# Optimization experiments

Measured on AMD Instinct MI355X. Metric: run time of the kernel, lower is better.

The kernel has to match this reference:

```python
import jax, jax.numpy as jnp
import numpy as np

CONFIDENCE = 0.1
EPS = 1e-3  # keras BatchNormalization default epsilon
B, H, W, C = 4, 64, 64, 256


def setup_inputs() -> dict:
    key = jax.random.key(0)
    ks = jax.random.split(key, 6)
    return {
        "x": jax.random.normal(ks[0], (B, H, W, C), jnp.float32),
        "ca_gamma": jnp.ones((C,), jnp.float32),
        "ca_beta": jnp.zeros((C,), jnp.float32),
        "ca_mean": jnp.zeros((C,), jnp.float32),
        "ca_var": jnp.ones((C,), jnp.float32),
        "wq": jax.random.normal(ks[1], (C, C), jnp.float32) * 0.05,
        "wk": jax.random.normal(ks[2], (C, C), jnp.float32) * 0.05,
        "wv": jax.random.normal(ks[3], (C, C), jnp.float32) * 0.05,
        "wp": jax.random.normal(ks[4], (C, C), jnp.float32) * 0.05,
        "bn_gamma": jnp.ones((C,), jnp.float32),
        "bn_beta": jnp.zeros((C,), jnp.float32),
        "bn_mean": jnp.zeros((C,), jnp.float32),
        "bn_var": jnp.ones((C,), jnp.float32),
        "w_qkv": jax.random.normal(ks[5], (C, 3), jnp.float32) * 0.05,
    }


def _bn(x, g, b, m, v):
    # keras BatchNormalization, inference mode
    return (x - m) * jax.lax.rsqrt(v + EPS) * g + b


def reference(x, ca_gamma, ca_beta, ca_mean, ca_var, wq, wk, wv, wp,
              bn_gamma, bn_beta, bn_mean, bn_var, w_qkv):
    b, h, w, c = x.shape
    # ---- ChannelAttention (TRACER Channel_Tracer; dropout = identity at inference) ----
    gap = x.mean(axis=(1, 2))                         # [B, C] global average pool
    gn = _bn(gap, ca_gamma, ca_beta, ca_mean, ca_var)  # [B, C]
    q = gn @ wq                                        # 1x1 conv on 1x1 map == matmul
    k = gn @ wk
    v = gn @ wv
    logits = q[:, :, None] * k[:, None, :]             # [B, C, C], head_dim = 1
    score = jax.nn.softmax(logits, axis=-1)
    att = jnp.einsum('bij,bj->bi', score, v)           # [B, C]
    cmask = jax.nn.sigmoid(att @ wp)                   # [B, C] channel mask (alpha)
    ca_out = x * cmask[:, None, None, :] + x           # residual channel re-weighting
    # ---- UnionAttention spatial part ----
    co = _bn(ca_out, bn_gamma, bn_beta, bn_mean, bn_var)
    thr = jnp.percentile(cmask, CONFIDENCE * 100.0, axis=-1,
                         keepdims=True, method='linear')  # [B, 1]
    pmask = jnp.where(cmask > thr, cmask, 0.0)          # percentile masking
    co = co * pmask[:, None, None, :]
    qkv = jnp.einsum('bhwc,cf->bhwf', co, w_qkv)        # [B, H, W, 3] fused q/k/v 1x1 conv
    n = h * w
    qs = qkv[..., 0].reshape(b, n)                      # [B, N], head_dim = 1
    ks_ = qkv[..., 1].reshape(b, n)
    vs = qkv[..., 2].reshape(b, n)
    sl = qs[:, :, None] * ks_[:, None, :]               # [B, N, N] scores (outer product)
    sw = jax.nn.softmax(sl, axis=-1)
    sa = jnp.einsum('bij,bj->bi', sw, vs)               # [B, N]
    return qkv[..., 2:3] + sa.reshape(b, h, w, 1)       # v + attention, [B, H, W, 1]
```

## Files before the change

### kernel.cpp

```cpp
#include <hip/hip_runtime.h>

#define EPS 1e-3f

#define OFF_PGAP   0
#define OFF_PART   65536
#define OFF_A      163840
#define OFF_BIAS   164864
#define OFF_QS     164880
#define OFF_KS     181264
#define OFF_VS     197648

__global__ __launch_bounds__(256) void k_gap(const float* __restrict__ x,
                                             const float* __restrict__ wq,
                                             const float* __restrict__ wk,
                                             const float* __restrict__ wv,
                                             const float* __restrict__ wp,
                                             float* __restrict__ pgap) {
    __shared__ float4 red[256];
    int blk = blockIdx.x;
    int t = threadIdx.x;

    const float* wmat = (blk < 64) ? wq : (blk < 128) ? wk : (blk < 192) ? wv : wp;
    float4 wv4 = *(const float4*)(wmat + (size_t)(blk & 63) * 1024 + 4 * t);

    int cg = t & 63;
    int pg = t >> 6;
    const float* xp = x + ((size_t)blk * 64 + pg * 16) * 256 + 4 * cg;
    float4 s = make_float4(0.f, 0.f, 0.f, 0.f);
    #pragma unroll
    for (int u = 0; u < 16; ++u) {
        float4 v = *(const float4*)(xp + (size_t)u * 256);
        s.x += v.x; s.y += v.y; s.z += v.z; s.w += v.w;
    }
    red[pg * 64 + cg] = s;
    asm volatile("" :: "v"(wv4.x), "v"(wv4.y), "v"(wv4.z), "v"(wv4.w));
    __syncthreads();
    if (t < 64) {
        float4 a = red[t], b4 = red[64 + t], c4 = red[128 + t], d4 = red[192 + t];
        float4 o = make_float4(a.x + b4.x + c4.x + d4.x,
                               a.y + b4.y + c4.y + d4.y,
                               a.z + b4.z + c4.z + d4.z,
                               a.w + b4.w + c4.w + d4.w);
        *(float4*)(pgap + blk * 256 + 4 * t) = o;
    }
}

__global__ __launch_bounds__(256) void k_qkvmat(
    const float* __restrict__ pgap,
    const float* __restrict__ cag, const float* __restrict__ cab,
    const float* __restrict__ cam, const float* __restrict__ cav,
    const float* __restrict__ wq, const float* __restrict__ wk,
    const float* __restrict__ wv,
    float* __restrict__ part)
{
    __shared__ float gpart[4][8][4];
    __shared__ float gn_s[4][8];
    int blk = blockIdx.x;
    int m = blk >> 5;
    int g = blk & 31;
    int r0 = g * 8;
    int t = threadIdx.x;
    const float* W = (m == 0) ? wq : (m == 1) ? wk : wv;

    if (t < 128) {
        int b = t >> 5, row = (t >> 2) & 7, p = t & 3;
        const float* pgp = pgap + ((size_t)(b * 64 + p * 16)) * 256 + r0 + row;
        float s = 0.f;
        #pragma unroll
        for (int ch = 0; ch < 16; ++ch) s += pgp[(size_t)ch * 256];
        gpart[b][row][p] = s;
    }
    __syncthreads();
    if (t < 32) {
        int b = t >> 3, row = t & 7;
        float gsum = gpart[b][row][0] + gpart[b][row][1]
                   + gpart[b][row][2] + gpart[b][row][3];
        float gv = gsum * (1.0f / 4096.0f);
        int c = r0 + row;
        float sc = cag[c] * rsqrtf(cav[c] + EPS);
        gn_s[b][row] = gv * sc + (cab[c] - cam[c] * sc);
    }
    __syncthreads();

    float a0 = 0.f, a1 = 0.f, a2 = 0.f, a3 = 0.f;
    const float* wp_ = W + (size_t)r0 * 256 + t;
    #pragma unroll
    for (int row = 0; row < 8; ++row) {
        float w = wp_[(size_t)row * 256];
        a0 = fmaf(gn_s[0][row], w, a0);
        a1 = fmaf(gn_s[1][row], w, a1);
        a2 = fmaf(gn_s[2][row], w, a2);
        a3 = fmaf(gn_s[3][row], w, a3);
    }
    float* o = part + (size_t)(m * 32 + g) * 1024 + t;
    o[0] = a0; o[256] = a1; o[512] = a2; o[768] = a3;
}

__global__ __launch_bounds__(512) void k_mid(
    const float* __restrict__ part,
    const float* __restrict__ wp,
    const float* __restrict__ bng, const float* __restrict__ bnb,
    const float* __restrict__ bnm, const float* __restrict__ bnv,
    const float* __restrict__ wqkv,
    float* __restrict__ Aout, float* __restrict__ biasOut)
{
    __shared__ float sq[256], sk[256], sv[256], att[256], cm[256], Bc[256];
    __shared__ float red[2048];
    __shared__ float swqkv[768];
    __shared__ float t25, t26, thr;

    int b = blockIdx.x;
    int t = threadIdx.x;
    int cg = t & 63;
    int rg = t >> 6;
    int c4 = cg * 4;

    if (t < 384) {
        swqkv[t] = wqkv[t];
        swqkv[t + 384] = wqkv[t + 384];
    }

    {
        int m = t >> 8, c = t & 255;
        const float* p = part + (size_t)m * 32768 + b * 256 + c;
        float s = 0.f;
        #pragma unroll
        for (int g2 = 0; g2 < 32; ++g2) s += p[(size_t)g2 * 1024];
        if (m == 0) sq[c] = s; else sk[c] = s;
        if (t < 256) {
            const float* p2 = part + (size_t)2 * 32768 + b * 256 + t;
            float s2 = 0.f;
            #pragma unroll
            for (int g2 = 0; g2 < 32; ++g2) s2 += p2[(size_t)g2 * 1024];
            sv[t] = s2;
        }
    }
    __syncthreads();

    {
        int h = t >> 8, c = t & 255;
        float a = sq[c];
        int jb = h * 128;
        float mx = -1e30f;
        #pragma unroll 8
        for (int j = 0; j < 128; ++j) mx = fmaxf(mx, a * sk[jb + j]);
        float den = 0.f, num = 0.f;
        #pragma unroll 4
        for (int j = 0; j < 128; ++j) {
            float e = __expf(a * sk[jb + j] - mx);
            den += e; num = fmaf(e, sv[jb + j], num);
        }
        red[h * 256 + c] = mx;
        red[512 + h * 256 + c] = den;
        red[1024 + h * 256 + c] = num;
    }
    __syncthreads();
    if (t < 256) {
        float m0 = red[t], m1 = red[256 + t];
        float M = fmaxf(m0, m1);
        float s0 = __expf(m0 - M), s1 = __expf(m1 - M);
        float den = red[512 + t] * s0 + red[768 + t] * s1;
        float num = red[1024 + t] * s0 + red[1280 + t] * s1;
        att[t] = num / den;
    }
    __syncthreads();

    {
        int rbase = rg * 32;
        float4 ac = make_float4(0.f, 0.f, 0.f, 0.f);
        const float* wpp = wp + (size_t)rbase * 256 + c4;
        #pragma unroll 8
        for (int i = 0; i < 32; ++i) {
            float g = att[rbase + i];
            float4 w = *(const float4*)(wpp + (size_t)i * 256);
            ac.x = fmaf(g, w.x, ac.x); ac.y = fmaf(g, w.y, ac.y);
            ac.z = fmaf(g, w.z, ac.z); ac.w = fmaf(g, w.w, ac.w);
        }
        *(float4*)(red + rg * 256 + c4) = ac;
    }
    __syncthreads();
    if (t < 256) {
        float ac = 0.f;
        #pragma unroll
        for (int r = 0; r < 8; ++r) ac += red[r * 256 + t];
        cm[t] = 1.0f / (1.0f + __expf(-ac));
    }
    __syncthreads();

    if (t < 256) {
        float my = cm[t];
        int rank = 0;
        for (int j = 0; j < 256; ++j) {
            float o = cm[j];
            rank += (o < my) ? 1 : ((o == my && j < t) ? 1 : 0);
        }
        if (rank == 25) t25 = my;
        if (rank == 26) t26 = my;
    }
    __syncthreads();
    if (t == 0) thr = t25 + 0.5f * (t26 - t25);
    __syncthreads();

    if (t < 256) {
        float s2 = bng[t] * rsqrtf(bnv[t] + EPS);
        float o2 = bnb[t] - bnm[t] * s2;
        float cc = cm[t];
        float pm = (cc > thr) ? cc : 0.f;
        Aout[b * 256 + t] = (1.f + cc) * s2 * pm;
        Bc[t] = o2 * pm;
    }
    __syncthreads();
    if (t < 3) {
        float s3 = 0.f;
        for (int ch = 0; ch < 256; ++ch) s3 = fmaf(Bc[ch], swqkv[ch * 3 + t], s3);
        biasOut[b * 3 + t] = s3;
    }
}

__global__ __launch_bounds__(256) void k_qkv(
    const float* __restrict__ x, const float* __restrict__ A,
    const float* __restrict__ wqkv, const float* __restrict__ bias,
    float* __restrict__ qs, float* __restrict__ ks, float* __restrict__ vs)
{
    int lane = threadIdx.x & 63;
    int wid = (blockIdx.x * 256 + threadIdx.x) >> 6;
    float4 wA = *(const float4*)(wqkv + 12 * lane);
    float4 wB = *(const float4*)(wqkv + 12 * lane + 4);
    float4 wC = *(const float4*)(wqkv + 12 * lane + 8);
    float w00 = wA.x, w01 = wA.y, w02 = wA.z;
    float w10 = wA.w, w11 = wB.x, w12 = wB.y;
    float w20 = wB.z, w21 = wB.w, w22 = wC.x;
    float w30 = wC.y, w31 = wC.z, w32 = wC.w;
    #pragma unroll
    for (int b = 0; b < 4; ++b) {
        int pix = b * 4096 + wid;
        float4 xv = *(const float4*)(x + (size_t)pix * 256 + 4 * lane);
        float4 A4 = *(const float4*)(A + b * 256 + 4 * lane);
        float t0 = xv.x * A4.x, t1 = xv.y * A4.y;
        float t2 = xv.z * A4.z, t3 = xv.w * A4.w;
        float q = t0 * w00 + t1 * w10 + t2 * w20 + t3 * w30;
        float k = t0 * w01 + t1 * w11 + t2 * w21 + t3 * w31;
        float v = t0 * w02 + t1 * w12 + t2 * w22 + t3 * w32;
        #pragma unroll
        for (int m = 1; m < 64; m <<= 1) {
            q += __shfl_xor(q, m, 64);
            k += __shfl_xor(k, m, 64);
            v += __shfl_xor(v, m, 64);
        }
        if (lane == 0) {
            qs[pix] = q + bias[b * 3 + 0];
            ks[pix] = k + bias[b * 3 + 1];
            vs[pix] = v + bias[b * 3 + 2];
        }
    }
}

__global__ __launch_bounds__(512) void k_attn2(
    const float* __restrict__ qs, const float* __restrict__ ks, const float* __restrict__ vs,
    float* __restrict__ out)
{
    __shared__ float4 skv[2048];
    __shared__ float pden[8][64], pnum[8][64];
    __shared__ float rmax[8], rmin[8];
    int blk = blockIdx.x;
    int b = blk >> 6, ic = blk & 63;
    int t = threadIdx.x;
    int lane = t & 63, sub = t >> 6;
    int base = b * 4096;

    const float4* k4 = (const float4*)(ks + base);
    const float4* v4 = (const float4*)(vs + base);
    float kmx = -1e30f, kmn = 1e30f;
    #pragma unroll
    for (int u = 0; u < 2; ++u) {
        int i = t + u * 512;
        float4 kk = k4[i], vv = v4[i];
        skv[i * 2]     = make_float4(kk.x, vv.x, kk.y, vv.y);
        skv[i * 2 + 1] = make_float4(kk.z, vv.z, kk.w, vv.w);
        kmx = fmaxf(kmx, fmaxf(fmaxf(kk.x, kk.y), fmaxf(kk.z, kk.w)));
        kmn = fminf(kmn, fminf(fminf(kk.x, kk.y), fminf(kk.z, kk.w)));
    }
    #pragma unroll
    for (int m2 = 1; m2 < 64; m2 <<= 1) {
        kmx = fmaxf(kmx, __shfl_xor(kmx, m2, 64));
        kmn = fminf(kmn, __shfl_xor(kmn, m2, 64));
    }
    if (lane == 0) { rmax[sub] = kmx; rmin[sub] = kmn; }
    __syncthreads();
    float mx = rmax[0], mn = rmin[0];
    #pragma unroll
    for (int s = 1; s < 8; ++s) { mx = fmaxf(mx, rmax[s]); mn = fminf(mn, rmin[s]); }

    int row = ic * 64 + lane;
    float a = qs[base + row];
    float m = (a >= 0.f) ? a * mx : a * mn;
    float den0 = 0.f, num0 = 0.f, den1 = 0.f, num1 = 0.f;
    const float4* sp = skv + sub * 256;
    #pragma unroll 4
    for (int j = 0; j < 256; ++j) {
        float4 kv = sp[j];
        float e0 = __expf(fmaf(a, kv.x, -m));
        float e1 = __expf(fmaf(a, kv.z, -m));
        den0 += e0; num0 = fmaf(e0, kv.y, num0);
        den1 += e1; num1 = fmaf(e1, kv.w, num1);
    }
    pden[sub][lane] = den0 + den1;
    pnum[sub][lane] = num0 + num1;
    __syncthreads();
    if (t < 64) {
        float den = 0.f, num = 0.f;
        #pragma unroll
        for (int s = 0; s < 8; ++s) { den += pden[s][t]; num += pnum[s][t]; }
        int r = ic * 64 + t;
        float vrow = (r & 1) ? skv[r >> 1].w : skv[r >> 1].y;
        out[base + r] = vrow + num / den;
    }
}

extern "C" void kernel_launch(void* const* d_in, const int* in_sizes, int n_in,
                              void* d_out, int out_size, void* d_ws, size_t ws_size,
                              hipStream_t stream) {
    const float* x    = (const float*)d_in[0];
    const float* cag  = (const float*)d_in[1];
    const float* cab  = (const float*)d_in[2];
    const float* cam  = (const float*)d_in[3];
    const float* cav  = (const float*)d_in[4];
    const float* wq   = (const float*)d_in[5];
    const float* wk   = (const float*)d_in[6];
    const float* wv   = (const float*)d_in[7];
    const float* wp   = (const float*)d_in[8];
    const float* bng  = (const float*)d_in[9];
    const float* bnb  = (const float*)d_in[10];
    const float* bnm  = (const float*)d_in[11];
    const float* bnv  = (const float*)d_in[12];
    const float* wqkv = (const float*)d_in[13];

    float* ws   = (float*)d_ws;
    float* pgap = ws + OFF_PGAP;
    float* part = ws + OFF_PART;
    float* A    = ws + OFF_A;
    float* bias = ws + OFF_BIAS;
    float* qs   = ws + OFF_QS;
    float* ks   = ws + OFF_KS;
    float* vs   = ws + OFF_VS;

    k_gap<<<dim3(256), dim3(256), 0, stream>>>(x, wq, wk, wv, wp, pgap);
    k_qkvmat<<<dim3(96), dim3(256), 0, stream>>>(pgap, cag, cab, cam, cav,
                                                 wq, wk, wv, part);
    k_mid<<<dim3(4), dim3(512), 0, stream>>>(part, wp, bng, bnb, bnm, bnv, wqkv,
                                             A, bias);
    k_qkv<<<dim3(1024), dim3(256), 0, stream>>>(x, A, wqkv, bias, qs, ks, vs);
    k_attn2<<<dim3(256), dim3(512), 0, stream>>>(qs, ks, vs, (float*)d_out);
}
```

Measured before the change: 137.0 us.

## Widen early kernels to 512 threads and use analytic softmax max in channel attention

The GAP kernel now uses 512 threads with 8 rows each and also prefetches the BN parameter vectors into cache. The q/k/v matvec kernel splits rows across two thread halves with a shared-memory reduction, and writes its partials in a layout that can be read with float2 loads. The channel softmax replaces the per-row max scan and two-half rescaling with a closed-form row max taken from the global max/min of k. Together these shorten the serial critical path of the small tail kernels, at the cost of extra syncs and shared memory.

```diff
diff --git a/kernel.cpp b/kernel.cpp
--- a/kernel.cpp
+++ b/kernel.cpp
@@ -4,48 +4,63 @@
 
 #define OFF_PGAP   0
 #define OFF_PART   65536
-#define OFF_A      163840
+#define OFF_AW     163840
 #define OFF_BIAS   164864
 #define OFF_QS     164880
 #define OFF_KS     181264
 #define OFF_VS     197648
 
-__global__ __launch_bounds__(256) void k_gap(const float* __restrict__ x,
-                                             const float* __restrict__ wq,
-                                             const float* __restrict__ wk,
-                                             const float* __restrict__ wv,
-                                             const float* __restrict__ wp,
-                                             float* __restrict__ pgap) {
-    __shared__ float4 red[256];
+__global__ __launch_bounds__(512) void k_gap(
+    const float* __restrict__ x,
+    const float* __restrict__ wq, const float* __restrict__ wk,
+    const float* __restrict__ wv, const float* __restrict__ wp,
+    const float* __restrict__ bng, const float* __restrict__ bnb,
+    const float* __restrict__ bnm, const float* __restrict__ bnv,
+    const float* __restrict__ cag, const float* __restrict__ cab,
+    const float* __restrict__ cam, const float* __restrict__ cav,
+    float* __restrict__ pgap)
+{
+    __shared__ float4 s4[512];
     int blk = blockIdx.x;
     int t = threadIdx.x;
-
-    const float* wmat = (blk < 64) ? wq : (blk < 128) ? wk : (blk < 192) ? wv : wp;
-    float4 wv4 = *(const float4*)(wmat + (size_t)(blk & 63) * 1024 + 4 * t);
-
-    int cg = t & 63;
-    int pg = t >> 6;
-    const float* xp = x + ((size_t)blk * 64 + pg * 16) * 256 + 4 * cg;
+    int lane = t & 63, sub = t >> 6;
+
+    if (t < 256) {
+        const float* wmat = (blk < 64) ? wq : (blk < 128) ? wk
+                          : (blk < 192) ? wv : wp;
+        float4 w4 = *(const float4*)(wmat + (size_t)(blk & 63) * 1024 + 4 * t);
+        asm volatile("" :: "v"(w4.x), "v"(w4.y), "v"(w4.z), "v"(w4.w));
+    }
+    if (blk == 1 && t < 256) {
+        float z = bng[t] + bnb[t] + bnm[t] + bnv[t];
+        asm volatile("" :: "v"(z));
+    }
+    if (blk == 2 && t < 256) {
+        float z = cag[t] + cab[t] + cam[t] + cav[t];
+        asm volatile("" :: "v"(z));
+    }
+
+    const float* xp = x + ((size_t)blk * 64 + sub * 8) * 256 + 4 * lane;
     float4 s = make_float4(0.f, 0.f, 0.f, 0.f);
     #pragma unroll
-    for (int u = 0; u < 16; ++u) {
+    for (int u = 0; u < 8; ++u) {
         float4 v = *(const float4*)(xp + (size_t)u * 256);
         s.x += v.x; s.y += v.y; s.z += v.z; s.w += v.w;
     }
-    red[pg * 64 + cg] = s;
-    asm volatile("" :: "v"(wv4.x), "v"(wv4.y), "v"(wv4.z), "v"(wv4.w));
+    s4[sub * 64 + lane] = s;
     __syncthreads();
     if (t < 64) {
-        float4 a = red[t], b4 = red[64 + t], c4 = red[128 + t], d4 = red[192 + t];
-        float4 o = make_float4(a.x + b4.x + c4.x + d4.x,
-                               a.y + b4.y + c4.y + d4.y,
-                               a.z + b4.z + c4.z + d4.z,
-                               a.w + b4.w + c4.w + d4.w);
+        float4 o = s4[t];
+        #pragma unroll
+        for (int p = 1; p < 8; ++p) {
+            float4 v = s4[p * 64 + t];
+            o.x += v.x; o.y += v.y; o.z += v.z; o.w += v.w;
+        }
         *(float4*)(pgap + blk * 256 + 4 * t) = o;
     }
 }
 
-__global__ __launch_bounds__(256) void k_qkvmat(
+__global__ __launch_bounds__(512) void k_qkvmat(
     const float* __restrict__ pgap,
     const float* __restrict__ cag, const float* __restrict__ cab,
     const float* __restrict__ cam, const float* __restrict__ cav,
@@ -53,125 +68,136 @@
     const float* __restrict__ wv,
     float* __restrict__ part)
 {
-    __shared__ float gpart[4][8][4];
-    __shared__ float gn_s[4][8];
+    __shared__ float gpart[512];
+    __shared__ float gn_s[32];
+    __shared__ float red[2048];
     int blk = blockIdx.x;
-    int m = blk >> 5;
-    int g = blk & 31;
+    int m = blk / 32, g = blk % 32;
     int r0 = g * 8;
     int t = threadIdx.x;
     const float* W = (m == 0) ? wq : (m == 1) ? wk : wv;
 
-    if (t < 128) {
-        int b = t >> 5, row = (t >> 2) & 7, p = t & 3;
-        const float* pgp = pgap + ((size_t)(b * 64 + p * 16)) * 256 + r0 + row;
+    {
+        int b = t >> 7, row = (t >> 4) & 7, p4 = t & 15;
         float s = 0.f;
         #pragma unroll
-        for (int ch = 0; ch < 16; ++ch) s += pgp[(size_t)ch * 256];
-        gpart[b][row][p] = s;
+        for (int q = 0; q < 4; ++q)
+            s += pgap[(size_t)(b * 64 + p4 * 4 + q) * 256 + r0 + row];
+        gpart[b * 128 + row * 16 + p4] = s;
     }
     __syncthreads();
     if (t < 32) {
         int b = t >> 3, row = t & 7;
-        float gsum = gpart[b][row][0] + gpart[b][row][1]
-                   + gpart[b][row][2] + gpart[b][row][3];
-        float gv = gsum * (1.0f / 4096.0f);
+        float s = 0.f;
+        #pragma unroll
+        for (int p = 0; p < 16; ++p) s += gpart[b * 128 + row * 16 + p];
+        float gv = s * (1.0f / 4096.0f);
         int c = r0 + row;
         float sc = cag[c] * rsqrtf(cav[c] + EPS);
-        gn_s[b][row] = gv * sc + (cab[c] - cam[c] * sc);
-    }
-    __syncthreads();
-
-    float a0 = 0.f, a1 = 0.f, a2 = 0.f, a3 = 0.f;
-    const float* wp_ = W + (size_t)r0 * 256 + t;
-    #pragma unroll
-    for (int row = 0; row < 8; ++row) {
-        float w = wp_[(size_t)row * 256];
-        a0 = fmaf(gn_s[0][row], w, a0);
-        a1 = fmaf(gn_s[1][row], w, a1);
-        a2 = fmaf(gn_s[2][row], w, a2);
-        a3 = fmaf(gn_s[3][row], w, a3);
-    }
-    float* o = part + (size_t)(m * 32 + g) * 1024 + t;
-    o[0] = a0; o[256] = a1; o[512] = a2; o[768] = a3;
+        gn_s[b * 8 + row] = gv * sc + (cab[c] - cam[c] * sc);
+    }
+    __syncthreads();
+    {
+        int c = t & 255, h = t >> 8;
+        float a0 = 0.f, a1 = 0.f, a2 = 0.f, a3 = 0.f;
+        #pragma unroll
+        for (int rr = 0; rr < 4; ++rr) {
+            int ri = h * 4 + rr;
+            float w = W[(size_t)(r0 + ri) * 256 + c];
+            a0 = fmaf(gn_s[0 * 8 + ri], w, a0);
+            a1 = fmaf(gn_s[1 * 8 + ri], w, a1);
+            a2 = fmaf(gn_s[2 * 8 + ri], w, a2);
+            a3 = fmaf(gn_s[3 * 8 + ri], w, a3);
+        }
+        red[(h * 4 + 0) * 256 + c] = a0;
+        red[(h * 4 + 1) * 256 + c] = a1;
+        red[(h * 4 + 2) * 256 + c] = a2;
+        red[(h * 4 + 3) * 256 + c] = a3;
+    }
+    __syncthreads();
+    {
+        int b = t >> 7, c0 = (t & 127) * 2;
+        float v0 = red[b * 256 + c0]     + red[(4 + b) * 256 + c0];
+        float v1 = red[b * 256 + c0 + 1] + red[(4 + b) * 256 + c0 + 1];
+        *(float2*)(part + (size_t)((m * 32 + g) * 4 + b) * 256 + c0) =
+            make_float2(v0, v1);
+    }
 }
 
 __global__ __launch_bounds__(512) void k_mid(
-    const float* __restrict__ part,
-    const float* __restrict__ wp,
+    const float* __restrict__ part, const float* __restrict__ wp,
     const float* __restrict__ bng, const float* __restrict__ bnb,
     const float* __restrict__ bnm, const float* __restrict__ bnv,
     const float* __restrict__ wqkv,
-    float* __restrict__ Aout, float* __restrict__ biasOut)
-{
-    __shared__ float sq[256], sk[256], sv[256], att[256], cm[256], Bc[256];
+    float* __restrict__ Aw, float* __restrict__ biasW)
+{
+    __shared__ float sq[256], sk[256], sv[256], att[256], cmv[256], Bc[256];
     __shared__ float red[2048];
-    __shared__ float swqkv[768];
-    __shared__ float t25, t26, thr;
-
+    __shared__ float swq[768];
+    __shared__ float sc2[8];
     int b = blockIdx.x;
     int t = threadIdx.x;
-    int cg = t & 63;
-    int rg = t >> 6;
-    int c4 = cg * 4;
+    int lane = t & 63, sub = t >> 6;
+
+    if (t < 384) { swq[t] = wqkv[t]; swq[t + 384] = wqkv[t + 384]; }
 
     if (t < 384) {
-        swqkv[t] = wqkv[t];
-        swqkv[t + 384] = wqkv[t + 384];
-    }
-
-    {
-        int m = t >> 8, c = t & 255;
-        const float* p = part + (size_t)m * 32768 + b * 256 + c;
-        float s = 0.f;
-        #pragma unroll
-        for (int g2 = 0; g2 < 32; ++g2) s += p[(size_t)g2 * 1024];
-        if (m == 0) sq[c] = s; else sk[c] = s;
-        if (t < 256) {
-            const float* p2 = part + (size_t)2 * 32768 + b * 256 + t;
-            float s2 = 0.f;
-            #pragma unroll
-            for (int g2 = 0; g2 < 32; ++g2) s2 += p2[(size_t)g2 * 1024];
-            sv[t] = s2;
-        }
-    }
-    __syncthreads();
-
-    {
-        int h = t >> 8, c = t & 255;
+        int m = t >> 7, c0 = (t & 127) * 2;
+        float a0 = 0.f, a1 = 0.f;
+        #pragma unroll 8
+        for (int g = 0; g < 32; ++g) {
+            float2 v = *(const float2*)(part +
+                          (size_t)((m * 32 + g) * 4 + b) * 256 + c0);
+            a0 += v.x; a1 += v.y;
+        }
+        float* dst = (m == 0) ? sq : (m == 1) ? sk : sv;
+        dst[c0] = a0; dst[c0 + 1] = a1;
+    }
+    __syncthreads();
+
+    if (t < 64) {
+        float mx = -1e30f, mn = 1e30f;
+        #pragma unroll
+        for (int u = 0; u < 4; ++u) {
+            float v = sk[t + u * 64];
+            mx = fmaxf(mx, v); mn = fminf(mn, v);
+        }
+        #pragma unroll
+        for (int m2 = 1; m2 < 64; m2 <<= 1) {
+            mx = fmaxf(mx, __shfl_xor(mx, m2, 64));
+            mn = fminf(mn, __shfl_xor(mn, m2, 64));
+        }
+        if (t == 0) { sc2[0] = mx; sc2[1] = mn; }
+    }
+    __syncthreads();
+
+    {
+        int c = t & 255, h = t >> 8;
         float a = sq[c];
-        int jb = h * 128;
-        float mx = -1e30f;
-        #pragma unroll 8
-        for (int j = 0; j < 128; ++j) mx = fmaxf(mx, a * sk[jb + j]);
+        float m = (a >= 0.f) ? a * sc2[0] : a * sc2[1];
+        const float* skp = sk + h * 128;
+        const float* svp = sv + h * 128;
         float den = 0.f, num = 0.f;
         #pragma unroll 4
         for (int j = 0; j < 128; ++j) {
-            float e = __expf(a * sk[jb + j] - mx);
-            den += e; num = fmaf(e, sv[jb + j], num);
-        }
-        red[h * 256 + c] = mx;
-        red[512 + h * 256 + c] = den;
-        red[1024 + h * 256 + c] = num;
-    }
-    __syncthreads();
-    if (t < 256) {
-        float m0 = red[t], m1 = red[256 + t];
-        float M = fmaxf(m0, m1);
-        float s0 = __expf(m0 - M), s1 = __expf(m1 - M);
-        float den = red[512 + t] * s0 + red[768 + t] * s1;
-        float num = red[1024 + t] * s0 + red[1280 + t] * s1;
-        att[t] = num / den;
-    }
-    __syncthreads();
-
-    {
-        int rbase = rg * 32;
+            float e = __expf(fmaf(a, skp[j], -m));
+            den += e; num = fmaf(e, svp[j], num);
+        }
+        red[h * 256 + c] = den;
+        red[512 + h * 256 + c] = num;
+    }
+    __syncthreads();
+    if (t < 256)
+        att[t] = (red[512 + t] + red[768 + t]) / (red[t] + red[256 + t]);
+    __syncthreads();
+
+    {
+        int rg = sub, c4 = lane * 4;
         float4 ac = make_float4(0.f, 0.f, 0.f, 0.f);
-        const float* wpp = wp + (size_t)rbase * 256 + c4;
+        const float* wpp = wp + (size_t)rg * 32 * 256 + c4;
         #pragma unroll 8
         for (int i = 0; i < 32; ++i) {
-            float g = att[rbase + i];
+            float g = att[rg * 32 + i];
             float4 w = *(const float4*)(wpp + (size_t)i * 256);
             ac.x = fmaf(g, w.x, ac.x); ac.y = fmaf(g, w.y, ac.y);
             ac.z = fmaf(g, w.z, ac.z); ac.w = fmaf(g, w.w, ac.w);
@@ -183,37 +209,38 @@
         float ac = 0.f;
         #pragma unroll
         for (int r = 0; r < 8; ++r) ac += red[r * 256 + t];
-        cm[t] = 1.0f / (1.0f + __expf(-ac));
+        cmv[t] = 1.0f / (1.0f + __expf(-ac));
     }
     __syncthreads();
 
     if (t < 256) {
-        float my = cm[t];
+        float my = cmv[t];
         int rank = 0;
         for (int j = 0; j < 256; ++j) {
-            float o = cm[j];
+            float o = cmv[j];
             rank += (o < my) ? 1 : ((o == my && j < t) ? 1 : 0);
         }
-        if (rank == 25) t25 = my;
-        if (rank == 26) t26 = my;
-    }
-    __syncthreads();
-    if (t == 0) thr = t25 + 0.5f * (t26 - t25);
+        if (rank == 25) sc2[2] = my;
+        if (rank == 26) sc2[3] = my;
+    }
+    __syncthreads();
+    if (t == 0) sc2[4] = sc2[2] + 0.5f * (sc2[3] - sc2[2]);
     __syncthreads();
 
     if (t < 256) {
         float s2 = bng[t] * rsqrtf(bnv[t] + EPS);
         float o2 = bnb[t] - bnm[t] * s2;
-        float cc = cm[t];
-        float pm = (cc > thr) ? cc : 0.f;
-        Aout[b * 256 + t] = (1.f + cc) * s2 * pm;
+        float cc = cmv[t];
+        float pm = (cc > sc2[4]) ? cc : 0.f;
+        Aw[b * 256 + t] = (1.f + cc) * s2 * pm;
         Bc[t] = o2 * pm;
     }
     __syncthreads();
     if (t < 3) {
         float s3 = 0.f;
-        for (int ch = 0; ch < 256; ++ch) s3 = fmaf(Bc[ch], swqkv[ch * 3 + t], s3);
-        biasOut[b * 3 + t] = s3;
+        for (int ch = 0; ch < 256; ++ch)
+            s3 = fmaf(Bc[ch], swq[ch * 3 + t], s3);
+        biasW[b * 3 + t] = s3;
     }
 }
 
@@ -256,8 +283,8 @@
 }
 
 __global__ __launch_bounds__(512) void k_attn2(
-    const float* __restrict__ qs, const float* __restrict__ ks, const float* __restrict__ vs,
-    float* __restrict__ out)
+    const float* __restrict__ qs, const float* __restrict__ ks,
+    const float* __restrict__ vs, float* __restrict__ out)
 {
     __shared__ float4 skv[2048];
     __shared__ float pden[8][64], pnum[8][64];
@@ -338,17 +365,19 @@
     float* ws   = (float*)d_ws;
     float* pgap = ws + OFF_PGAP;
     float* part = ws + OFF_PART;
-    float* A    = ws + OFF_A;
+    float* Aw   = ws + OFF_AW;
     float* bias = ws + OFF_BIAS;
     float* qs   = ws + OFF_QS;
     float* ks   = ws + OFF_KS;
     float* vs   = ws + OFF_VS;
 
-    k_gap<<<dim3(256), dim3(256), 0, stream>>>(x, wq, wk, wv, wp, pgap);
-    k_qkvmat<<<dim3(96), dim3(256), 0, stream>>>(pgap, cag, cab, cam, cav,
+    k_gap<<<dim3(256), dim3(512), 0, stream>>>(x, wq, wk, wv, wp,
+                                               bng, bnb, bnm, bnv,
+                                               cag, cab, cam, cav, pgap);
+    k_qkvmat<<<dim3(96), dim3(512), 0, stream>>>(pgap, cag, cab, cam, cav,
                                                  wq, wk, wv, part);
-    k_mid<<<dim3(4), dim3(512), 0, stream>>>(part, wp, bng, bnb, bnm, bnv, wqkv,
-                                             A, bias);
-    k_qkv<<<dim3(1024), dim3(256), 0, stream>>>(x, A, wqkv, bias, qs, ks, vs);
+    k_mid<<<dim3(4), dim3(512), 0, stream>>>(part, wp, bng, bnb, bnm, bnv,
+                                             wqkv, Aw, bias);
+    k_qkv<<<dim3(1024), dim3(256), 0, stream>>>(x, Aw, wqkv, bias, qs, ks, vs);
     k_attn2<<<dim3(256), dim3(512), 0, stream>>>(qs, ks, vs, (float*)d_out);
 }
```

Measured after the change: 130.5 us. -4.7%, faster.
